# Kernel tuning notes

Measured on AMD Instinct MI355X. Metric: run time of the kernel, lower is better.

Reference implementation:

```python
import jax, jax.numpy as jnp
import numpy as np
import math

B, S, D = 16, 1024, 512
ALPHA = 1.0
DIRECTION = 'fw'


def masked_softmax(vec, mask):
    # faithful to the torch helper: multiply-by-mask, max-shift, exp, re-mask, normalize
    masked_vec = vec * mask
    max_vec = jnp.max(masked_vec, axis=2, keepdims=True)
    exps = jnp.exp(masked_vec - max_vec)
    masked_exps = exps * mask
    masked_sums = jnp.sum(masked_exps, axis=2, keepdims=True)
    masked_sums = masked_sums + (masked_sums == 0).astype(vec.dtype)
    return masked_exps / (masked_sums + 1e-20)


def setup_inputs() -> dict:
    key = jax.random.key(0)
    kq, kk, kv, km = jax.random.split(key, 4)
    q = jax.random.normal(kq, (B, S, D), dtype=jnp.float32)
    k = jax.random.normal(kk, (B, S, D), dtype=jnp.float32)
    v = jax.random.normal(kv, (B, S, D), dtype=jnp.float32)
    rep_mask = jax.random.randint(km, (B, S, 1), 0, 2, dtype=jnp.int32)
    return {"q": q, "k": k, "v": v, "rep_mask": rep_mask}


def reference(q, k, v, rep_mask):
    seq_len = q.shape[1]
    scale = jnp.asarray(math.sqrt(D), dtype=q.dtype)
    attention = jnp.einsum('bqd,bkd->bqk', q, k) / scale  # [B,S,S]

    ones = jnp.ones((seq_len, seq_len), dtype=q.dtype)
    if DIRECTION == 'fw':
        dir_mask = jnp.tril(ones, k=-1)
    else:
        dir_mask = jnp.triu(ones, k=1)

    rm = rep_mask.astype(q.dtype)                     # [B,S,1]
    rep = rm * jnp.swapaxes(rm, 1, 2)                 # [B,S,S]

    idx = jnp.arange(seq_len)
    dis_mask = -jnp.abs(idx[:, None] - idx[None, :]).astype(q.dtype)  # [S,S]

    mask = rep * dir_mask[None]                       # [B,S,S]
    attention = attention + ALPHA * dis_mask[None]
    attention = masked_softmax(attention, mask)
    out = jnp.einsum('bqk,bkd->bqd', attention, v)
    return (out, attention)
```

## Files before the change

### kernel.cpp

```cpp
#include <hip/hip_runtime.h>
#include <cstdint>

#define B_ 16
#define S_ 1024
#define D_ 512
#define TILE 128
#define BK 32
#define PITCH 36

typedef float f32x4 __attribute__((ext_vector_type(4)));
typedef short s16x8 __attribute__((ext_vector_type(8)));
typedef unsigned short u16;
typedef unsigned int u32;

__device__ __forceinline__ u16 f2bf(float f) {
    u32 u = __builtin_bit_cast(u32, f);
    u += 0x7FFFu + ((u >> 16) & 1u);
    return (u16)(u >> 16);
}

#define GLD16(g, l) __builtin_amdgcn_global_load_lds( \
    (const __attribute__((address_space(1))) u32*)(g), \
    (__attribute__((address_space(3))) u32*)(l), 16, 0, 0)

#define TP 66
__global__ __launch_bounds__(256) void prep_kernel(const float* __restrict__ q,
                                                   const float* __restrict__ k,
                                                   const float* __restrict__ v,
                                                   u16* __restrict__ Qb,
                                                   u16* __restrict__ Kb,
                                                   u16* __restrict__ Vt) {
    __shared__ u16 t[64 * TP];
    const int bid = blockIdx.x;
    const int tid = threadIdx.x;
    if (bid < 8192) {
        const float* src = (bid < 4096) ? q : k;
        u16* dst = (bid < 4096) ? Qb : Kb;
        int i = (((bid & 4095) * 256) + tid) * 8;
        float4 a = *(const float4*)(src + i);
        float4 b2 = *(const float4*)(src + i + 4);
        union { ushort4 h[2]; s16x8 v; } r;
        r.h[0] = make_ushort4(f2bf(a.x), f2bf(a.y), f2bf(a.z), f2bf(a.w));
        r.h[1] = make_ushort4(f2bf(b2.x), f2bf(b2.y), f2bf(b2.z), f2bf(b2.w));
        *(s16x8*)(dst + i) = r.v;
    } else {
        int tt = bid - 8192;
        const int d0 = (tt & 7) * 64, j0 = ((tt >> 3) & 15) * 64, b = tt >> 7;
        const int tj = tid >> 2;
        const int td = (tid & 3) * 16;
        const float* src = v + ((size_t)b * S_ + j0 + tj) * D_ + d0 + td;
#pragma unroll
        for (int e = 0; e < 4; ++e) {
            float4 a = *(const float4*)(src + e * 4);
            *(ushort4*)(t + tj * TP + td + e * 4) =
                make_ushort4(f2bf(a.x), f2bf(a.y), f2bf(a.z), f2bf(a.w));
        }
        __syncthreads();
        const int dd = tid >> 2;
        const int jj = (tid & 3) * 16;
        u16* dstp = Vt + ((size_t)b * D_ + d0 + dd) * S_ + j0 + jj;
        u16 tmp[16];
#pragma unroll
        for (int e = 0; e < 16; ++e) tmp[e] = t[(jj + e) * TP + dd];
        *(s16x8*)dstp = *(s16x8*)tmp;
        *(s16x8*)(dstp + 8) = *(s16x8*)(tmp + 8);
    }
}

__device__ __forceinline__ s16x8 frag_swz(const u16* lds, int row, int colbyte) {
    int off = row * 128 + (colbyte ^ ((row & 7) << 4));
    return *(const s16x8*)((const char*)lds + off);
}

__device__ __forceinline__ void gemm_body(const u16* ag, const u16* bg, int lda, int ldb,
                                          int nk, u16* lA, u16* lB, f32x4 acc[4][4],
                                          int tid) {
    const int lane = tid & 63, wid = tid >> 6;
    const int l8 = lane >> 3, l7 = lane & 7;
    const int cswz = (l7 ^ l8) * 8;
    const u16* ga[4];
    const u16* gb[4];
#pragma unroll
    for (int q2 = 0; q2 < 4; ++q2) {
        int seg = wid * 4 + q2;
        int row = seg * 8 + l8;
        ga[q2] = ag + (size_t)row * lda + cswz;
        gb[q2] = bg + (size_t)row * ldb + cswz;
    }
    const int wr = (wid >> 1) * 64, wc = (wid & 1) * 64;
    const int r15 = lane & 15;
    const int cb = (lane >> 4) * 16;

    for (int kk = 0; kk < nk; kk += 64) {
#pragma unroll
        for (int q2 = 0; q2 < 4; ++q2) {
            int seg = wid * 4 + q2;
            GLD16(ga[q2] + kk, lA + seg * 512);
            GLD16(gb[q2] + kk, lB + seg * 512);
        }
        __syncthreads();
#pragma unroll
        for (int ks = 0; ks < 2; ++ks) {
            s16x8 af[4], bf4[4];
#pragma unroll
            for (int m = 0; m < 4; ++m) af[m] = frag_swz(lA, wr + m * 16 + r15, ks * 64 + cb);
#pragma unroll
            for (int n = 0; n < 4; ++n) bf4[n] = frag_swz(lB, wc + n * 16 + r15, ks * 64 + cb);
#pragma unroll
            for (int m = 0; m < 4; ++m)
#pragma unroll
                for (int n = 0; n < 4; ++n)
                    acc[m][n] = __builtin_amdgcn_mfma_f32_16x16x32_bf16(af[m], bf4[n], acc[m][n], 0, 0, 0);
        }
        __syncthreads();
    }
}

__global__ __launch_bounds__(256) void qk2_kernel(const u16* __restrict__ Qb,
                                                  const u16* __restrict__ Kb,
                                                  const int* __restrict__ rep,
                                                  float* __restrict__ attn) {
    const int bid = blockIdx.x;
    const int xcd = bid & 7;
    const int w = bid >> 3;
    const int b = xcd * 2 + (w & 1);
    int p = 35 - (w >> 1);
    int qt = 0, tri = 0;
    while (p >= tri + qt + 1) { tri += qt + 1; ++qt; }
    const int kt = p - tri;

    __shared__ u16 lA[128 * 64];
    __shared__ u16 lB[128 * 64];
    __shared__ int lrepr[128];
    const int tid = threadIdx.x, lane = tid & 63, wid = tid >> 6;
    if (tid < 128) lrepr[tid] = rep[(size_t)b * S_ + qt * 128 + tid];

    f32x4 acc[4][4] = {};
    gemm_body(Qb + ((size_t)b * S_ + (size_t)qt * 128) * D_,
              Kb + ((size_t)b * S_ + (size_t)kt * 128) * D_,
              D_, D_, D_, lA, lB, acc, tid);
    const float scale = 0.04419417382415922f;
    const int wr = (wid >> 1) * 64, wc = (wid & 1) * 64;
    const int r15 = lane & 15, rr = (lane >> 4) * 4;
    size_t base = ((size_t)b * S_ + (size_t)qt * 128) * S_ + (size_t)kt * 128;
#pragma unroll
    for (int m = 0; m < 4; ++m)
#pragma unroll
        for (int r = 0; r < 4; ++r) {
            const int row = wr + m * 16 + rr + r;
            if (lrepr[row]) {
#pragma unroll
                for (int n = 0; n < 4; ++n)
                    attn[base + (size_t)row * S_ + wc + n * 16 + r15] =
                        acc[m][n][r] * scale;
            }
        }
}

__global__ __launch_bounds__(256) void pv2_kernel(const u16* __restrict__ Pb,
                                                  const u16* __restrict__ Vt,
                                                  float* __restrict__ out) {
    const int bid = blockIdx.x;
    const int xcd = bid & 7;
    const int w = bid >> 3;
    const int b = xcd * 2 + (w & 1);
    const int r = w >> 1;
    const int dt = r & 3, qt = 7 - (r >> 2);

    __shared__ u16 lA[128 * 64];
    __shared__ u16 lB[128 * 64];
    const int tid = threadIdx.x, lane = tid & 63, wid = tid >> 6;
    f32x4 acc[4][4] = {};
    gemm_body(Pb + ((size_t)b * S_ + (size_t)qt * 128) * S_,
              Vt + ((size_t)b * D_ + (size_t)dt * 128) * S_,
              S_, S_, (qt + 1) * 128, lA, lB, acc, tid);
    const int wr = (wid >> 1) * 64, wc = (wid & 1) * 64;
    const int r15 = lane & 15, rr = (lane >> 4) * 4;
    size_t base = ((size_t)b * S_ + (size_t)qt * 128) * D_ + (size_t)dt * 128;
#pragma unroll
    for (int m = 0; m < 4; ++m)
#pragma unroll
        for (int n = 0; n < 4; ++n)
#pragma unroll
            for (int rg = 0; rg < 4; ++rg)
                out[base + (size_t)(wr + m * 16 + rr + rg) * D_ + wc + n * 16 + r15] =
                    acc[m][n][rg];
}

__global__ __launch_bounds__(256) void sm_kernel(const int* __restrict__ rep_mask,
                                                 float* __restrict__ attn,
                                                 u16* __restrict__ pb) {
    const int i = blockIdx.x, b = blockIdx.y;
    const int tid = threadIdx.x;
    const int lane = tid & 63, wid = tid >> 6;
    float* row = attn + ((size_t)b * S_ + i) * S_;
    const int* rm = rep_mask + (size_t)b * S_;
    __shared__ float red[8];

    const int mi = rm[i];
    const int j0 = tid * 4;
    int4 m4 = ((const int4*)rm)[tid];
    float4 lv = make_float4(0.f, 0.f, 0.f, 0.f);
    if (mi != 0 && j0 < i) lv = *(const float4*)(row + j0);

    const int mv[4] = {m4.x, m4.y, m4.z, m4.w};
    const float lf[4] = {lv.x, lv.y, lv.z, lv.w};
    float vec[4];
    bool val[4];
    float mymax = 0.0f;
#pragma unroll
    for (int e = 0; e < 4; ++e) {
        int j = j0 + e;
        val[e] = (mi != 0) && (j < i) && (mv[e] != 0);
        vec[e] = lf[e] - (float)(i - j);
        if (val[e]) mymax = fmaxf(mymax, vec[e]);
    }
#pragma unroll
    for (int off = 32; off > 0; off >>= 1) mymax = fmaxf(mymax, __shfl_down(mymax, off));
    if (lane == 0) red[wid] = mymax;
    __syncthreads();
    const float m = fmaxf(fmaxf(red[0], red[1]), fmaxf(red[2], red[3]));

    float ex[4];
    float mysum = 0.0f;
#pragma unroll
    for (int e = 0; e < 4; ++e) {
        ex[e] = val[e] ? expf(vec[e] - m) : 0.0f;
        mysum += ex[e];
    }
#pragma unroll
    for (int off = 32; off > 0; off >>= 1) mysum += __shfl_down(mysum, off);
    if (lane == 0) red[4 + wid] = mysum;
    __syncthreads();
    const float ssum = red[4] + red[5] + red[6] + red[7];
    const float denom = ssum + (ssum == 0.0f ? 1.0f : 0.0f) + 1e-20f;
    const float inv = 1.0f / denom;
    float4 o = make_float4(ex[0] * inv, ex[1] * inv, ex[2] * inv, ex[3] * inv);
    *(float4*)(row + j0) = o;
    if (pb != nullptr && j0 <= (i | 127)) {
        u16* pr = pb + ((size_t)b * S_ + i) * S_ + j0;
        *(ushort4*)pr = make_ushort4(f2bf(o.x), f2bf(o.y), f2bf(o.z), f2bf(o.w));
    }
}


union Frag { s16x8 v; uint2 u[2]; };

__device__ __forceinline__ s16x8 load_frag(const u16* lds, int row, int kq) {
    Frag f;
    const u16* p = lds + row * PITCH + kq;
    f.u[0] = *(const uint2*)p;
    f.u[1] = *(const uint2*)(p + 4);
    return f.v;
}

__device__ __forceinline__ void stage_granule(u16* lds, const float* src, int ldsrc, int g) {
    int row = g >> 2;
    int c8 = (g & 3) * 8;
    const float4* s = (const float4*)(src + (size_t)row * ldsrc + c8);
    float4 x0 = s[0], x1 = s[1];
    *(ushort4*)(lds + row * PITCH + c8) =
        make_ushort4(f2bf(x0.x), f2bf(x0.y), f2bf(x0.z), f2bf(x0.w));
    *(ushort4*)(lds + row * PITCH + c8 + 4) =
        make_ushort4(f2bf(x1.x), f2bf(x1.y), f2bf(x1.z), f2bf(x1.w));
}

__global__ __launch_bounds__(256) void qk_kernel(const float* __restrict__ q,
                                                 const float* __restrict__ k,
                                                 float* __restrict__ attn) {
    const int kt = blockIdx.x, qt = blockIdx.y, b = blockIdx.z;
    if (kt > qt) return;
    __shared__ u16 lA[TILE * PITCH];
    __shared__ u16 lB[TILE * PITCH];
    const int tid = threadIdx.x;
    const int lane = tid & 63;
    const int wid = tid >> 6;
    const int wr = (wid >> 1) * 64, wc = (wid & 1) * 64;
    const int r15 = lane & 15, kq = (lane >> 4) * 8;
    const float* qb = q + ((size_t)b * S_ + (size_t)qt * TILE) * D_;
    const float* kb = k + ((size_t)b * S_ + (size_t)kt * TILE) * D_;
    f32x4 acc[4][4] = {};
    for (int kk = 0; kk < D_; kk += BK) {
        __syncthreads();
        stage_granule(lA, qb + kk, D_, tid);
        stage_granule(lA, qb + kk, D_, tid + 256);
        stage_granule(lB, kb + kk, D_, tid);
        stage_granule(lB, kb + kk, D_, tid + 256);
        __syncthreads();
        s16x8 af[4], bf[4];
#pragma unroll
        for (int m = 0; m < 4; ++m) af[m] = load_frag(lA, wr + m * 16 + r15, kq);
#pragma unroll
        for (int n = 0; n < 4; ++n) bf[n] = load_frag(lB, wc + n * 16 + r15, kq);
#pragma unroll
        for (int m = 0; m < 4; ++m)
#pragma unroll
            for (int n = 0; n < 4; ++n)
                acc[m][n] = __builtin_amdgcn_mfma_f32_16x16x32_bf16(af[m], bf[n], acc[m][n], 0, 0, 0);
    }
    const float scale = 0.04419417382415922f;
    size_t base = ((size_t)b * S_ + (size_t)qt * TILE) * S_ + (size_t)kt * TILE;
    const int rr = (lane >> 4) * 4;
#pragma unroll
    for (int m = 0; m < 4; ++m)
#pragma unroll
        for (int n = 0; n < 4; ++n)
#pragma unroll
            for (int r = 0; r < 4; ++r)
                attn[base + (size_t)(wr + m * 16 + rr + r) * S_ + wc + n * 16 + r15] =
                    acc[m][n][r] * scale;
}

__global__ __launch_bounds__(256) void pv_kernel(const float* __restrict__ attn,
                                                 const float* __restrict__ v,
                                                 float* __restrict__ out) {
    const int dt = blockIdx.x, qt = blockIdx.y, b = blockIdx.z;
    __shared__ u16 lP[TILE * PITCH];
    __shared__ u16 lV[TILE * PITCH];
    const int tid = threadIdx.x;
    const int lane = tid & 63;
    const int wid = tid >> 6;
    const int wr = (wid >> 1) * 64, wc = (wid & 1) * 64;
    const int r15 = lane & 15, kq = (lane >> 4) * 8;
    const float* pb = attn + ((size_t)b * S_ + (size_t)qt * TILE) * S_;
    const float* vb = v + (size_t)b * S_ * D_ + (size_t)dt * TILE;
    const int vd0 = (tid & 31) * 4;
    const int vj0 = (tid >> 5) * 4;
    f32x4 acc[4][4] = {};
    const int nk = (qt + 1) * TILE;
    for (int kk = 0; kk < nk; kk += BK) {
        __syncthreads();
        stage_granule(lP, pb + kk, S_, tid);
        stage_granule(lP, pb + kk, S_, tid + 256);
        {
            const float* vs = vb + (size_t)(kk + vj0) * D_ + vd0;
            float4 r0 = *(const float4*)vs;
            float4 r1 = *(const float4*)(vs + D_);
            float4 r2 = *(const float4*)(vs + 2 * D_);
            float4 r3 = *(const float4*)(vs + 3 * D_);
            *(ushort4*)(lV + (vd0 + 0) * PITCH + vj0) = make_ushort4(f2bf(r0.x), f2bf(r1.x), f2bf(r2.x), f2bf(r3.x));
            *(ushort4*)(lV + (vd0 + 1) * PITCH + vj0) = make_ushort4(f2bf(r0.y), f2bf(r1.y), f2bf(r2.y), f2bf(r3.y));
            *(ushort4*)(lV + (vd0 + 2) * PITCH + vj0) = make_ushort4(f2bf(r0.z), f2bf(r1.z), f2bf(r2.z), f2bf(r3.z));
            *(ushort4*)(lV + (vd0 + 3) * PITCH + vj0) = make_ushort4(f2bf(r0.w), f2bf(r1.w), f2bf(r2.w), f2bf(r3.w));
        }
        __syncthreads();
        s16x8 af[4], bf[4];
#pragma unroll
        for (int m = 0; m < 4; ++m) af[m] = load_frag(lP, wr + m * 16 + r15, kq);
#pragma unroll
        for (int n = 0; n < 4; ++n) bf[n] = load_frag(lV, wc + n * 16 + r15, kq);
#pragma unroll
        for (int m = 0; m < 4; ++m)
#pragma unroll
            for (int n = 0; n < 4; ++n)
                acc[m][n] = __builtin_amdgcn_mfma_f32_16x16x32_bf16(af[m], bf[n], acc[m][n], 0, 0, 0);
    }
    size_t base = ((size_t)b * S_ + (size_t)qt * TILE) * D_ + (size_t)dt * TILE;
    const int rr = (lane >> 4) * 4;
#pragma unroll
    for (int m = 0; m < 4; ++m)
#pragma unroll
        for (int n = 0; n < 4; ++n)
#pragma unroll
            for (int r = 0; r < 4; ++r)
                out[base + (size_t)(wr + m * 16 + rr + r) * D_ + wc + n * 16 + r15] =
                    acc[m][n][r];
}

extern "C" void kernel_launch(void* const* d_in, const int* in_sizes, int n_in,
                              void* d_out, int out_size, void* d_ws, size_t ws_size,
                              hipStream_t stream) {
    const float* q = (const float*)d_in[0];
    const float* k = (const float*)d_in[1];
    const float* v = (const float*)d_in[2];
    const int* rep = (const int*)d_in[3];
    float* out = (float*)d_out;
    float* attn = out + (size_t)B_ * S_ * D_;

    const size_t nqk = (size_t)B_ * S_ * D_;
    const size_t need = 3 * nqk * sizeof(u16);
    if (ws_size >= need) {
        u16* Qb = (u16*)d_ws;
        u16* Kb = Qb + nqk;
        u16* Vt = Kb + nqk;
        u16* Pb = (u16*)d_ws;
        prep_kernel<<<10240, 256, 0, stream>>>(q, k, v, Qb, Kb, Vt);
        qk2_kernel<<<8 * 72, 256, 0, stream>>>(Qb, Kb, rep, attn);
        sm_kernel<<<dim3(S_, B_), 256, 0, stream>>>(rep, attn, Pb);
        pv2_kernel<<<8 * 64, 256, 0, stream>>>(Pb, Vt, out);
    } else {
        qk_kernel<<<dim3(S_ / TILE, S_ / TILE, B_), 256, 0, stream>>>(q, k, attn);
        sm_kernel<<<dim3(S_, B_), 256, 0, stream>>>(rep, attn, nullptr);
        pv_kernel<<<dim3(D_ / TILE, S_ / TILE, B_), 256, 0, stream>>>(attn, v, out);
    }
}
```

Before: 90.05 us.

## Fuse softmax into QK and PV kernels with per-tile stats and bf16 P

The separate softmax kernel goes away. The QK kernel now computes per-tile row max and sum and writes unnormalized exp probabilities as packed triangular bf16. The PV kernel merges the tile stats, rescales P while staging it into LDS, writes the fp32 attention output from the dt==0 blocks, and zero-fills the upper region. Q conversion moves into the QK kernel's load path. This removes a full fp32 attention read/write round trip and one launch, at the cost of extra register and LDS work and bf16 rounding of P before normalisation.

Result: slower. 125.9 us (+39.8%).

```diff
diff --git a/kernel.cpp b/kernel.cpp
--- a/kernel.cpp
+++ b/kernel.cpp
@@ -18,33 +18,37 @@
     u += 0x7FFFu + ((u >> 16) & 1u);
     return (u16)(u >> 16);
 }
+__device__ __forceinline__ float bf2f(u16 h) {
+    return __builtin_bit_cast(float, (u32)h << 16);
+}
 
 #define GLD16(g, l) __builtin_amdgcn_global_load_lds( \
     (const __attribute__((address_space(1))) u32*)(g), \
     (__attribute__((address_space(3))) u32*)(l), 16, 0, 0)
 
+#define PT_BATCH 589824
+__device__ __forceinline__ int tri128(int qt) {
+    return ((qt * (qt + 1)) >> 1) * 16384;
+}
+
 #define TP 66
-__global__ __launch_bounds__(256) void prep_kernel(const float* __restrict__ q,
-                                                   const float* __restrict__ k,
-                                                   const float* __restrict__ v,
-                                                   u16* __restrict__ Qb,
-                                                   u16* __restrict__ Kb,
-                                                   u16* __restrict__ Vt) {
+__global__ __launch_bounds__(256) void prep2_kernel(const float* __restrict__ k,
+                                                    const float* __restrict__ v,
+                                                    u16* __restrict__ Kb,
+                                                    u16* __restrict__ Vt) {
     __shared__ u16 t[64 * TP];
     const int bid = blockIdx.x;
     const int tid = threadIdx.x;
-    if (bid < 8192) {
-        const float* src = (bid < 4096) ? q : k;
-        u16* dst = (bid < 4096) ? Qb : Kb;
-        int i = (((bid & 4095) * 256) + tid) * 8;
-        float4 a = *(const float4*)(src + i);
-        float4 b2 = *(const float4*)(src + i + 4);
+    if (bid < 4096) {
+        int i = ((bid * 256) + tid) * 8;
+        float4 a = *(const float4*)(k + i);
+        float4 b2 = *(const float4*)(k + i + 4);
         union { ushort4 h[2]; s16x8 v; } r;
         r.h[0] = make_ushort4(f2bf(a.x), f2bf(a.y), f2bf(a.z), f2bf(a.w));
         r.h[1] = make_ushort4(f2bf(b2.x), f2bf(b2.y), f2bf(b2.z), f2bf(b2.w));
-        *(s16x8*)(dst + i) = r.v;
+        *(s16x8*)(Kb + i) = r.v;
     } else {
-        int tt = bid - 8192;
+        int tt = bid - 4096;
         const int d0 = (tt & 7) * 64, j0 = ((tt >> 3) & 15) * 64, b = tt >> 7;
         const int tj = tid >> 2;
         const int td = (tid & 3) * 16;
@@ -72,54 +76,11 @@
     return *(const s16x8*)((const char*)lds + off);
 }
 
-__device__ __forceinline__ void gemm_body(const u16* ag, const u16* bg, int lda, int ldb,
-                                          int nk, u16* lA, u16* lB, f32x4 acc[4][4],
-                                          int tid) {
-    const int lane = tid & 63, wid = tid >> 6;
-    const int l8 = lane >> 3, l7 = lane & 7;
-    const int cswz = (l7 ^ l8) * 8;
-    const u16* ga[4];
-    const u16* gb[4];
-#pragma unroll
-    for (int q2 = 0; q2 < 4; ++q2) {
-        int seg = wid * 4 + q2;
-        int row = seg * 8 + l8;
-        ga[q2] = ag + (size_t)row * lda + cswz;
-        gb[q2] = bg + (size_t)row * ldb + cswz;
-    }
-    const int wr = (wid >> 1) * 64, wc = (wid & 1) * 64;
-    const int r15 = lane & 15;
-    const int cb = (lane >> 4) * 16;
-
-    for (int kk = 0; kk < nk; kk += 64) {
-#pragma unroll
-        for (int q2 = 0; q2 < 4; ++q2) {
-            int seg = wid * 4 + q2;
-            GLD16(ga[q2] + kk, lA + seg * 512);
-            GLD16(gb[q2] + kk, lB + seg * 512);
-        }
-        __syncthreads();
-#pragma unroll
-        for (int ks = 0; ks < 2; ++ks) {
-            s16x8 af[4], bf4[4];
-#pragma unroll
-            for (int m = 0; m < 4; ++m) af[m] = frag_swz(lA, wr + m * 16 + r15, ks * 64 + cb);
-#pragma unroll
-            for (int n = 0; n < 4; ++n) bf4[n] = frag_swz(lB, wc + n * 16 + r15, ks * 64 + cb);
-#pragma unroll
-            for (int m = 0; m < 4; ++m)
-#pragma unroll
-                for (int n = 0; n < 4; ++n)
-                    acc[m][n] = __builtin_amdgcn_mfma_f32_16x16x32_bf16(af[m], bf4[n], acc[m][n], 0, 0, 0);
-        }
-        __syncthreads();
-    }
-}
-
-__global__ __launch_bounds__(256) void qk2_kernel(const u16* __restrict__ Qb,
+__global__ __launch_bounds__(256) void qk3_kernel(const float* __restrict__ q,
                                                   const u16* __restrict__ Kb,
                                                   const int* __restrict__ rep,
-                                                  float* __restrict__ attn) {
+                                                  u16* __restrict__ Pt,
+                                                  float2* __restrict__ st) {
     const int bid = blockIdx.x;
     const int xcd = bid & 7;
     const int w = bid >> 3;
@@ -128,119 +89,245 @@
     int qt = 0, tri = 0;
     while (p >= tri + qt + 1) { tri += qt + 1; ++qt; }
     const int kt = p - tri;
+    const int nkq = (qt + 1) * 128;
 
     __shared__ u16 lA[128 * 64];
     __shared__ u16 lB[128 * 64];
     __shared__ int lrepr[128];
+    __shared__ int lrepc[128];
+    __shared__ float lst[2][64][2][2];
+
     const int tid = threadIdx.x, lane = tid & 63, wid = tid >> 6;
+    const int l8 = lane >> 3, l7 = lane & 7;
+    const int cswz = (l7 ^ l8) * 8;
+    const int r15 = lane & 15, g4 = lane >> 4;
+
     if (tid < 128) lrepr[tid] = rep[(size_t)b * S_ + qt * 128 + tid];
+    else lrepc[tid - 128] = rep[(size_t)b * S_ + kt * 128 + (tid - 128)];
+
+    const u16* bg = Kb + ((size_t)b * S_ + (size_t)kt * 128) * D_;
+    const u16* gb[4];
+#pragma unroll
+    for (int q2 = 0; q2 < 4; ++q2)
+        gb[q2] = bg + (size_t)((wid * 4 + q2) * 8 + l8) * D_ + cswz;
+
+    const float* ag = q + ((size_t)b * S_ + (size_t)qt * 128) * D_;
+    const int au = tid & 7;
+    const int ar0 = (tid >> 3) * 4;
 
     f32x4 acc[4][4] = {};
-    gemm_body(Qb + ((size_t)b * S_ + (size_t)qt * 128) * D_,
-              Kb + ((size_t)b * S_ + (size_t)kt * 128) * D_,
-              D_, D_, D_, lA, lB, acc, tid);
+    const int wr = (wid >> 1) * 64, wc = (wid & 1) * 64;
+    const int cb = g4 * 16;
+
+    for (int kk = 0; kk < D_; kk += 64) {
+#pragma unroll
+        for (int q2 = 0; q2 < 4; ++q2)
+            GLD16(gb[q2] + kk, lB + (wid * 4 + q2) * 512);
+#pragma unroll
+        for (int rr = 0; rr < 4; ++rr) {
+            int row = ar0 + rr;
+            const float* src = ag + (size_t)row * D_ + kk + au * 8;
+            float4 x0 = *(const float4*)src;
+            float4 x1 = *(const float4*)(src + 4);
+            union { ushort4 h[2]; s16x8 v; } rv;
+            rv.h[0] = make_ushort4(f2bf(x0.x), f2bf(x0.y), f2bf(x0.z), f2bf(x0.w));
+            rv.h[1] = make_ushort4(f2bf(x1.x), f2bf(x1.y), f2bf(x1.z), f2bf(x1.w));
+            *(s16x8*)(lA + row * 64 + (au ^ (row & 7)) * 8) = rv.v;
+        }
+        __syncthreads();
+#pragma unroll
+        for (int ks = 0; ks < 2; ++ks) {
+            s16x8 af[4], bf4[4];
+#pragma unroll
+            for (int m = 0; m < 4; ++m) af[m] = frag_swz(lA, wr + m * 16 + r15, ks * 64 + cb);
+#pragma unroll
+            for (int n = 0; n < 4; ++n) bf4[n] = frag_swz(lB, wc + n * 16 + r15, ks * 64 + cb);
+#pragma unroll
+            for (int m = 0; m < 4; ++m)
+#pragma unroll
+                for (int n = 0; n < 4; ++n)
+                    acc[m][n] = __builtin_amdgcn_mfma_f32_16x16x32_bf16(af[m], bf4[n], acc[m][n], 0, 0, 0);
+        }
+        __syncthreads();
+    }
+
     const float scale = 0.04419417382415922f;
-    const int wr = (wid >> 1) * 64, wc = (wid & 1) * 64;
-    const int r15 = lane & 15, rr = (lane >> 4) * 4;
-    size_t base = ((size_t)b * S_ + (size_t)qt * 128) * S_ + (size_t)kt * 128;
 #pragma unroll
     for (int m = 0; m < 4; ++m)
 #pragma unroll
         for (int r = 0; r < 4; ++r) {
-            const int row = wr + m * 16 + rr + r;
-            if (lrepr[row]) {
-#pragma unroll
-                for (int n = 0; n < 4; ++n)
-                    attn[base + (size_t)row * S_ + wc + n * 16 + r15] =
-                        acc[m][n][r] * scale;
+            const int rowl = m * 16 + g4 * 4 + r;
+            const int row = wr + rowl;
+            const int gi = qt * 128 + row;
+            const int im = lrepr[row];
+            float mx = 0.0f;
+#pragma unroll
+            for (int n = 0; n < 4; ++n) {
+                const int col = wc + n * 16 + r15;
+                const int gj = kt * 128 + col;
+                if (im && (gj < gi) && (lrepc[col] != 0))
+                    mx = fmaxf(mx, acc[m][n][r] * scale - (float)(gi - gj));
             }
-        }
-}
-
-__global__ __launch_bounds__(256) void pv2_kernel(const u16* __restrict__ Pb,
-                                                  const u16* __restrict__ Vt,
-                                                  float* __restrict__ out) {
+#pragma unroll
+            for (int off = 1; off < 16; off <<= 1)
+                mx = fmaxf(mx, __shfl_xor(mx, off));
+            if (r15 == 0) lst[wid >> 1][rowl][wid & 1][0] = mx;
+        }
+    __syncthreads();
+
+    u16* ptb = Pt + (size_t)b * PT_BATCH + tri128(qt);
+#pragma unroll
+    for (int m = 0; m < 4; ++m)
+#pragma unroll
+        for (int r = 0; r < 4; ++r) {
+            const int rowl = m * 16 + g4 * 4 + r;
+            const int row = wr + rowl;
+            const int gi = qt * 128 + row;
+            const int im = lrepr[row];
+            const float Mt = fmaxf(lst[wid >> 1][rowl][0][0], lst[wid >> 1][rowl][1][0]);
+            float sm = 0.0f;
+#pragma unroll
+            for (int n = 0; n < 4; ++n) {
+                const int col = wc + n * 16 + r15;
+                const int gj = kt * 128 + col;
+                const bool val = im && (gj < gi) && (lrepc[col] != 0);
+                float pt = val ? __expf(acc[m][n][r] * scale - (float)(gi - gj) - Mt) : 0.0f;
+                sm += pt;
+                if (im) ptb[(size_t)row * nkq + kt * 128 + col] = f2bf(pt);
+            }
+#pragma unroll
+            for (int off = 1; off < 16; off <<= 1)
+                sm += __shfl_xor(sm, off);
+            if (r15 == 0) lst[wid >> 1][rowl][wid & 1][1] = sm;
+        }
+    __syncthreads();
+    if (tid < 128) {
+        const int half = tid >> 6, row64 = tid & 63;
+        float Mt = fmaxf(lst[half][row64][0][0], lst[half][row64][1][0]);
+        float S = lst[half][row64][0][1] + lst[half][row64][1][1];
+        st[(((size_t)b * 8 + kt) << 10) + qt * 128 + tid] = make_float2(Mt, S);
+    }
+}
+
+__global__ __launch_bounds__(256) void pvsm_kernel(const u16* __restrict__ Pt,
+                                                   const float2* __restrict__ st,
+                                                   const int* __restrict__ rep,
+                                                   const u16* __restrict__ Vt,
+                                                   float* __restrict__ attn,
+                                                   float* __restrict__ out) {
     const int bid = blockIdx.x;
-    const int xcd = bid & 7;
-    const int w = bid >> 3;
+    const int xcd = bid & 7, w = bid >> 3;
     const int b = xcd * 2 + (w & 1);
-    const int r = w >> 1;
-    const int dt = r & 3, qt = 7 - (r >> 2);
+    const int r_ = w >> 1;
+    const int dt = r_ & 3, qt = 7 - (r_ >> 2);
+    const int nk = (qt + 1) * 128;
 
     __shared__ u16 lA[128 * 64];
     __shared__ u16 lB[128 * 64];
+    __shared__ float lC[128][8];
+    __shared__ int lmi[128];
+
     const int tid = threadIdx.x, lane = tid & 63, wid = tid >> 6;
+    const int l8 = lane >> 3, l7 = lane & 7;
+    const int cswz = (l7 ^ l8) * 8;
+    const int r15 = lane & 15, g4 = lane >> 4;
+
+    if (tid < 128) {
+        const int gi = qt * 128 + tid;
+        float M = 0.0f, S = 0.0f;
+        for (int kt = 0; kt <= qt; ++kt) {
+            float2 ms = st[(((size_t)b * 8 + kt) << 10) + gi];
+            float Mn = fmaxf(M, ms.x);
+            S = S * __expf(M - Mn) + ms.y * __expf(ms.x - Mn);
+            M = Mn;
+        }
+        const float inv = 1.0f / ((S == 0.0f ? 1.0f : S) + 1e-20f);
+        for (int kt = 0; kt <= qt; ++kt) {
+            float2 ms = st[(((size_t)b * 8 + kt) << 10) + gi];
+            lC[tid][kt] = __expf(ms.x - M) * inv;
+        }
+        lmi[tid] = rep[(size_t)b * S_ + gi];
+    }
+    __syncthreads();
+
+    const u16* pts = Pt + (size_t)b * PT_BATCH + tri128(qt);
+    float* aw = attn + ((size_t)b * S_ + (size_t)qt * 128) * S_;
+    const u16* bg = Vt + ((size_t)b * D_ + (size_t)dt * 128) * S_;
+    const u16* gb[4];
+#pragma unroll
+    for (int q2 = 0; q2 < 4; ++q2)
+        gb[q2] = bg + (size_t)((wid * 4 + q2) * 8 + l8) * S_ + cswz;
+
+    const int au = tid & 7;
+    const int ar0 = (tid >> 3) * 4;
+
     f32x4 acc[4][4] = {};
-    gemm_body(Pb + ((size_t)b * S_ + (size_t)qt * 128) * S_,
-              Vt + ((size_t)b * D_ + (size_t)dt * 128) * S_,
-              S_, S_, (qt + 1) * 128, lA, lB, acc, tid);
     const int wr = (wid >> 1) * 64, wc = (wid & 1) * 64;
-    const int r15 = lane & 15, rr = (lane >> 4) * 4;
+    const int cb = g4 * 16;
+
+    for (int kk = 0; kk < nk; kk += 64) {
+#pragma unroll
+        for (int q2 = 0; q2 < 4; ++q2)
+            GLD16(gb[q2] + kk, lB + (wid * 4 + q2) * 512);
+#pragma unroll
+        for (int rr = 0; rr < 4; ++rr) {
+            int row = ar0 + rr;
+            float pf[8];
+            if (lmi[row]) {
+                union { s16x8 v; u16 h[8]; } pt;
+                pt.v = *(const s16x8*)(pts + (size_t)row * nk + kk + au * 8);
+                const float cc = lC[row][kk >> 7];
+#pragma unroll
+                for (int e = 0; e < 8; ++e) pf[e] = bf2f(pt.h[e]) * cc;
+            } else {
+#pragma unroll
+                for (int e = 0; e < 8; ++e) pf[e] = 0.0f;
+            }
+            union { ushort4 h[2]; s16x8 v; } rv;
+            rv.h[0] = make_ushort4(f2bf(pf[0]), f2bf(pf[1]), f2bf(pf[2]), f2bf(pf[3]));
+            rv.h[1] = make_ushort4(f2bf(pf[4]), f2bf(pf[5]), f2bf(pf[6]), f2bf(pf[7]));
+            *(s16x8*)(lA + row * 64 + (au ^ (row & 7)) * 8) = rv.v;
+            if (dt == 0) {
+                float* dst = aw + (size_t)row * S_ + kk + au * 8;
+                *(float4*)dst = make_float4(pf[0], pf[1], pf[2], pf[3]);
+                *(float4*)(dst + 4) = make_float4(pf[4], pf[5], pf[6], pf[7]);
+            }
+        }
+        __syncthreads();
+#pragma unroll
+        for (int ks = 0; ks < 2; ++ks) {
+            s16x8 af[4], bf4[4];
+#pragma unroll
+            for (int m = 0; m < 4; ++m) af[m] = frag_swz(lA, wr + m * 16 + r15, ks * 64 + cb);
+#pragma unroll
+            for (int n = 0; n < 4; ++n) bf4[n] = frag_swz(lB, wc + n * 16 + r15, ks * 64 + cb);
+#pragma unroll
+            for (int m = 0; m < 4; ++m)
+#pragma unroll
+                for (int n = 0; n < 4; ++n)
+                    acc[m][n] = __builtin_amdgcn_mfma_f32_16x16x32_bf16(af[m], bf4[n], acc[m][n], 0, 0, 0);
+        }
+        __syncthreads();
+    }
+
+    if (dt == 1) {
+        const int tail = S_ - nk;
+        for (int t2 = tid * 4; t2 < 128 * tail; t2 += 1024) {
+            int row = t2 / tail, c2 = t2 - row * tail;
+            *(float4*)(aw + (size_t)row * S_ + nk + c2) = make_float4(0.f, 0.f, 0.f, 0.f);
+        }
+    }
+
     size_t base = ((size_t)b * S_ + (size_t)qt * 128) * D_ + (size_t)dt * 128;
+    const int rr2 = (lane >> 4) * 4;
 #pragma unroll
     for (int m = 0; m < 4; ++m)
 #pragma unroll
         for (int n = 0; n < 4; ++n)
 #pragma unroll
-            for (int rg = 0; rg < 4; ++rg)
-                out[base + (size_t)(wr + m * 16 + rr + rg) * D_ + wc + n * 16 + r15] =
-                    acc[m][n][rg];
-}
-
-__global__ __launch_bounds__(256) void sm_kernel(const int* __restrict__ rep_mask,
-                                                 float* __restrict__ attn,
-                                                 u16* __restrict__ pb) {
-    const int i = blockIdx.x, b = blockIdx.y;
-    const int tid = threadIdx.x;
-    const int lane = tid & 63, wid = tid >> 6;
-    float* row = attn + ((size_t)b * S_ + i) * S_;
-    const int* rm = rep_mask + (size_t)b * S_;
-    __shared__ float red[8];
-
-    const int mi = rm[i];
-    const int j0 = tid * 4;
-    int4 m4 = ((const int4*)rm)[tid];
-    float4 lv = make_float4(0.f, 0.f, 0.f, 0.f);
-    if (mi != 0 && j0 < i) lv = *(const float4*)(row + j0);
-
-    const int mv[4] = {m4.x, m4.y, m4.z, m4.w};
-    const float lf[4] = {lv.x, lv.y, lv.z, lv.w};
-    float vec[4];
-    bool val[4];
-    float mymax = 0.0f;
-#pragma unroll
-    for (int e = 0; e < 4; ++e) {
-        int j = j0 + e;
-        val[e] = (mi != 0) && (j < i) && (mv[e] != 0);
-        vec[e] = lf[e] - (float)(i - j);
-        if (val[e]) mymax = fmaxf(mymax, vec[e]);
-    }
-#pragma unroll
-    for (int off = 32; off > 0; off >>= 1) mymax = fmaxf(mymax, __shfl_down(mymax, off));
-    if (lane == 0) red[wid] = mymax;
-    __syncthreads();
-    const float m = fmaxf(fmaxf(red[0], red[1]), fmaxf(red[2], red[3]));
-
-    float ex[4];
-    float mysum = 0.0f;
-#pragma unroll
-    for (int e = 0; e < 4; ++e) {
-        ex[e] = val[e] ? expf(vec[e] - m) : 0.0f;
-        mysum += ex[e];
-    }
-#pragma unroll
-    for (int off = 32; off > 0; off >>= 1) mysum += __shfl_down(mysum, off);
-    if (lane == 0) red[4 + wid] = mysum;
-    __syncthreads();
-    const float ssum = red[4] + red[5] + red[6] + red[7];
-    const float denom = ssum + (ssum == 0.0f ? 1.0f : 0.0f) + 1e-20f;
-    const float inv = 1.0f / denom;
-    float4 o = make_float4(ex[0] * inv, ex[1] * inv, ex[2] * inv, ex[3] * inv);
-    *(float4*)(row + j0) = o;
-    if (pb != nullptr && j0 <= (i | 127)) {
-        u16* pr = pb + ((size_t)b * S_ + i) * S_ + j0;
-        *(ushort4*)pr = make_ushort4(f2bf(o.x), f2bf(o.y), f2bf(o.z), f2bf(o.w));
-    }
+            for (int r = 0; r < 4; ++r)
+                out[base + (size_t)(wr + m * 16 + rr2 + r) * D_ + wc + n * 16 + r15] =
+                    acc[m][n][r];
 }
 
 
@@ -309,6 +396,53 @@
             for (int r = 0; r < 4; ++r)
                 attn[base + (size_t)(wr + m * 16 + rr + r) * S_ + wc + n * 16 + r15] =
                     acc[m][n][r] * scale;
+}
+
+__global__ __launch_bounds__(256) void sm_kernel(const int* __restrict__ rep_mask,
+                                                 float* __restrict__ attn) {
+    const int i = blockIdx.x, b = blockIdx.y;
+    const int tid = threadIdx.x;
+    const int lane = tid & 63, wid = tid >> 6;
+    float* row = attn + ((size_t)b * S_ + i) * S_;
+    const int* rm = rep_mask + (size_t)b * S_;
+    __shared__ float red[8];
+    const int mi = rm[i];
+    const int j0 = tid * 4;
+    int4 m4 = ((const int4*)rm)[tid];
+    float4 lv = make_float4(0.f, 0.f, 0.f, 0.f);
+    if (mi != 0 && j0 < i) lv = *(const float4*)(row + j0);
+    const int mv[4] = {m4.x, m4.y, m4.z, m4.w};
+    const float lf[4] = {lv.x, lv.y, lv.z, lv.w};
+    float vec[4];
+    bool val[4];
+    float mymax = 0.0f;
+#pragma unroll
+    for (int e = 0; e < 4; ++e) {
+        int j = j0 + e;
+        val[e] = (mi != 0) && (j < i) && (mv[e] != 0);
+        vec[e] = lf[e] - (float)(i - j);
+        if (val[e]) mymax = fmaxf(mymax, vec[e]);
+    }
+#pragma unroll
+    for (int off = 32; off > 0; off >>= 1) mymax = fmaxf(mymax, __shfl_down(mymax, off));
+    if (lane == 0) red[wid] = mymax;
+    __syncthreads();
+    const float m = fmaxf(fmaxf(red[0], red[1]), fmaxf(red[2], red[3]));
+    float ex[4];
+    float mysum = 0.0f;
+#pragma unroll
+    for (int e = 0; e < 4; ++e) {
+        ex[e] = val[e] ? expf(vec[e] - m) : 0.0f;
+        mysum += ex[e];
+    }
+#pragma unroll
+    for (int off = 32; off > 0; off >>= 1) mysum += __shfl_down(mysum, off);
+    if (lane == 0) red[4 + wid] = mysum;
+    __syncthreads();
+    const float ssum = red[4] + red[5] + red[6] + red[7];
+    const float denom = ssum + (ssum == 0.0f ? 1.0f : 0.0f) + 1e-20f;
+    const float inv = 1.0f / denom;
+    *(float4*)(row + j0) = make_float4(ex[0] * inv, ex[1] * inv, ex[2] * inv, ex[3] * inv);
 }
 
 __global__ __launch_bounds__(256) void pv_kernel(const float* __restrict__ attn,
@@ -378,19 +512,20 @@
     float* attn = out + (size_t)B_ * S_ * D_;
 
     const size_t nqk = (size_t)B_ * S_ * D_;
-    const size_t need = 3 * nqk * sizeof(u16);
+    const size_t npt = (size_t)B_ * PT_BATCH;
+    const size_t nst = (size_t)B_ * 8 * S_;
+    const size_t need = 2 * nqk * sizeof(u16) + npt * sizeof(u16) + nst * sizeof(float2);
     if (ws_size >= need) {
-        u16* Qb = (u16*)d_ws;
-        u16* Kb = Qb + nqk;
+        u16* Kb = (u16*)d_ws;
         u16* Vt = Kb + nqk;
-        u16* Pb = (u16*)d_ws;
-        prep_kernel<<<10240, 256, 0, stream>>>(q, k, v, Qb, Kb, Vt);
-        qk2_kernel<<<8 * 72, 256, 0, stream>>>(Qb, Kb, rep, attn);
-        sm_kernel<<<dim3(S_, B_), 256, 0, stream>>>(rep, attn, Pb);
-        pv2_kernel<<<8 * 64, 256, 0, stream>>>(Pb, Vt, out);
+        u16* Pt = Vt + nqk;
+        float2* st = (float2*)(Pt + npt);
+        prep2_kernel<<<6144, 256, 0, stream>>>(k, v, Kb, Vt);
+        qk3_kernel<<<8 * 72, 256, 0, stream>>>(q, Kb, rep, Pt, st);
+        pvsm_kernel<<<8 * 64, 256, 0, stream>>>(Pt, st, rep, Vt, attn, out);
     } else {
         qk_kernel<<<dim3(S_ / TILE, S_ / TILE, B_), 256, 0, stream>>>(q, k, attn);
-        sm_kernel<<<dim3(S_, B_), 256, 0, stream>>>(rep, attn, nullptr);
+        sm_kernel<<<dim3(S_, B_), 256, 0, stream>>>(rep, attn);
         pv_kernel<<<dim3(D_ / TILE, S_ / TILE, B_), 256, 0, stream>>>(attn, v, out);
     }
 }
```
